# Optimization experiments

Measured on AMD Instinct MI355X. Metric: run time of the kernel, lower is better.

## Reference

```python
import jax, jax.numpy as jnp
import numpy as np

B, T, C, H = 2, 2048, 2048, 16
HD = C // H  # 128


def setup_inputs() -> dict:
    key = jax.random.key(0)
    k1, k2, k3 = jax.random.split(key, 3)
    x = jax.random.normal(k1, (B, T, C), jnp.float32)
    qkv_w = jax.random.normal(k2, (3 * C, C), jnp.float32) / np.float32(np.sqrt(C))
    proj_w = jax.random.normal(k3, (C, C), jnp.float32) / np.float32(np.sqrt(C))
    past = jnp.zeros((B, H, 2, T, HD), jnp.float32)  # KV cache: [B,H,2,max_seq,hd]
    return {"x": x, "qkv_w": qkv_w, "proj_w": proj_w, "past": past, "past_len": 0}


def reference(x, qkv_w, proj_w, past, past_len):
    Bx, Tx, Cx = x.shape
    hd = Cx // H
    # qkv projection (no bias), then split heads: [B,T,3C] -> [B,T,3,H,hd] -> [B,H,T,hd] each
    qkv = jnp.einsum('btc,dc->btd', x, qkv_w).reshape(Bx, Tx, 3, H, hd)
    q = jnp.transpose(qkv[:, :, 0], (0, 2, 1, 3))
    k = jnp.transpose(qkv[:, :, 1], (0, 2, 1, 3))
    v = jnp.transpose(qkv[:, :, 2], (0, 2, 1, 3))
    # KV-cache write (functional scatter) then read back the valid prefix
    past = past.at[:, :, 0, past_len:past_len + Tx].set(k)
    past = past.at[:, :, 1, past_len:past_len + Tx].set(v)
    k = past[:, :, 0, :past_len + Tx]
    v = past[:, :, 1, :past_len + Tx]
    S = past_len + Tx
    scale = np.float32(1.0 / np.sqrt(hd))
    scores = jnp.einsum('bhqd,bhkd->bhqk', q, k) * scale  # [B,H,T,S]
    if Tx > 1:  # is_causal=T>1 in the torch module (past_len=0 on this path)
        mask = jnp.arange(S)[None, :] <= (jnp.arange(Tx)[:, None] + past_len)
        scores = jnp.where(mask, scores, jnp.float32(-jnp.inf))
    attn = jax.nn.softmax(scores, axis=-1)
    out = jnp.einsum('bhqk,bhkd->bhqd', attn, v)  # [B,H,T,hd]
    out = jnp.transpose(out, (0, 2, 1, 3)).reshape(Bx, Tx, Cx)
    return jnp.einsum('btc,dc->btd', out, proj_w)
```

## Files before the change

kernel.cpp:

```cpp
#include <hip/hip_runtime.h>

typedef __bf16 bf16x8 __attribute__((ext_vector_type(8)));
typedef float f32x4 __attribute__((ext_vector_type(4)));
typedef unsigned short u16x8 __attribute__((ext_vector_type(8)));

__device__ __forceinline__ unsigned short f2bf(float f) {
  return __builtin_bit_cast(unsigned short, (__bf16)f);
}

__device__ __forceinline__ void gload16(const void* g, void* l) {
  __builtin_amdgcn_global_load_lds((const __attribute__((address_space(1))) unsigned int*)g,
                                   (__attribute__((address_space(3))) unsigned int*)l,
                                   16, 0, 0);
}

template <int N>
__device__ __forceinline__ float rormax(float x) {
  int r = __builtin_amdgcn_update_dpp(0, __builtin_bit_cast(int, x), 0x120 + N, 0xF, 0xF, true);
  return fmaxf(x, __builtin_bit_cast(float, r));
}
template <int N>
__device__ __forceinline__ float rorsum(float x) {
  int r = __builtin_amdgcn_update_dpp(0, __builtin_bit_cast(int, x), 0x120 + N, 0xF, 0xF, true);
  return x + __builtin_bit_cast(float, r);
}
__device__ __forceinline__ float red16max(float x) {
  x = rormax<8>(x); x = rormax<4>(x); x = rormax<2>(x); return rormax<1>(x);
}
__device__ __forceinline__ float red16sum(float x) {
  x = rorsum<8>(x); x = rorsum<4>(x); x = rorsum<2>(x); return rorsum<1>(x);
}

__global__ __launch_bounds__(256)
void cvt3_f32_bf16(const float* __restrict__ s0, unsigned short* __restrict__ d0, int n0,
                   const float* __restrict__ s1, unsigned short* __restrict__ d1, int n1,
                   const float* __restrict__ s2, unsigned short* __restrict__ d2)
{
  int blk = blockIdx.x;
  const float* s; unsigned short* d;
  if (blk < n0)            { s = s0; d = d0; }
  else if (blk < n0 + n1)  { s = s1; d = d1; blk -= n0; }
  else                     { s = s2; d = d2; blk -= n0 + n1; }
  const size_t e = ((size_t)blk * 256 + threadIdx.x) * 8;
  const float4 a = *(const float4*)(s + e);
  const float4 b = *(const float4*)(s + e + 4);
  u16x8 v;
  v[0] = f2bf(a.x); v[1] = f2bf(a.y); v[2] = f2bf(a.z); v[3] = f2bf(a.w);
  v[4] = f2bf(b.x); v[5] = f2bf(b.y); v[6] = f2bf(b.z); v[7] = f2bf(b.w);
  *(u16x8*)(d + e) = v;
}

#define STG(XS, Xg, buf, half, kt)                                              \
  { gload16((Xg) + (size_t)((half)*128 + srow8) * K + (kt)*64 + scol,           \
            (XS) + (buf)*32768 + (half)*16384 + wid*1024);                      \
    gload16((Xg) + (size_t)((half)*128 + 64 + srow8) * K + (kt)*64 + scol,      \
            (XS) + (buf)*32768 + (half)*16384 + 8192 + wid*1024); }

#define LDA(buf, ih)                                                            \
  { _Pragma("unroll") for (int i = 0; i < 4; ++i) {                             \
      const int ro = (buf)*32768 + arow + ((ih)*64 + i*16)*128;                 \
      af[i][0] = *(const bf16x8*)(As + ro + cbs0);                              \
      af[i][1] = *(const bf16x8*)(As + ro + cbs1); } }

#define LDB(buf, jh, BF)                                                        \
  { _Pragma("unroll") for (int j = 0; j < 2; ++j) {                             \
      const int ro = (buf)*32768 + brow + (((jh)*2 + j)*16)*128;                \
      BF[j][0] = *(const bf16x8*)(Bs + ro + cbs0);                              \
      BF[j][1] = *(const bf16x8*)(Bs + ro + cbs1); } }

#define MM(ih, jh, BF)                                                          \
  { _Pragma("unroll") for (int i = 0; i < 4; ++i)                               \
    _Pragma("unroll") for (int j = 0; j < 2; ++j)                               \
    _Pragma("unroll") for (int kk = 0; kk < 2; ++kk)                            \
      acc[(ih)*4+i][(jh)*2+j] = __builtin_amdgcn_mfma_f32_16x16x32_bf16(        \
          af[i][kk], BF[j][kk], acc[(ih)*4+i][(jh)*2+j], 0, 0, 0); }

#define BAR1_12() { asm volatile("s_waitcnt lgkmcnt(8)" ::: "memory");          \
                    __builtin_amdgcn_s_barrier();                               \
                    asm volatile("s_waitcnt lgkmcnt(0)" ::: "memory");          \
                    __builtin_amdgcn_sched_barrier(0);                          \
                    __builtin_amdgcn_s_setprio(1); }
#define BAR1()    { __builtin_amdgcn_s_barrier();                               \
                    asm volatile("s_waitcnt lgkmcnt(0)" ::: "memory");          \
                    __builtin_amdgcn_sched_barrier(0);                          \
                    __builtin_amdgcn_s_setprio(1); }
#define BAR2()    { __builtin_amdgcn_s_setprio(0); __builtin_amdgcn_s_barrier(); }
#define BAR2V()   { __builtin_amdgcn_s_setprio(0);                              \
                    asm volatile("s_waitcnt vmcnt(4)" ::: "memory");            \
                    __builtin_amdgcn_s_barrier(); }

template <bool OUTBF16>
__global__ __launch_bounds__(512, 1)
void gemm256_bt(const unsigned short* __restrict__ Ap, const unsigned short* __restrict__ Bp,
                void* __restrict__ Outp, int M, int N, int K)
{
  extern __shared__ __align__(16) char smem[];
  char* const As = smem;
  char* const Bs = smem + 65536;
  const int tid = threadIdx.x;
  const int wid = tid >> 6, lane = tid & 63;
  const int wm = wid >> 2, wn = wid & 3;
  const int lg = lane >> 4, lr = lane & 15;

  const int gx = gridDim.x;
  const int nwg = gx * (int)gridDim.y;
  int bid = (int)blockIdx.y * gx + (int)blockIdx.x;
  bid = (bid & 7) * (nwg >> 3) + (bid >> 3);
  const int m0 = (bid / gx) * 256, n0 = (bid % gx) * 256;

  const int srow8 = wid * 8 + (lane >> 3);
  const int scol  = (((lane & 7) ^ (lane >> 3)) << 3);
  const unsigned short* const Ag = Ap + (size_t)m0 * K;
  const unsigned short* const Bg = Bp + (size_t)n0 * K;

  const int cbs0 = (lg * 16) ^ ((lr & 7) << 4);
  const int cbs1 = (64 + lg * 16) ^ ((lr & 7) << 4);
  const int arow = (wm * 128 + lr) * 128;
  const int brow = (wn * 64 + lr) * 128;

  const f32x4 z4 = {0.f, 0.f, 0.f, 0.f};
  f32x4 acc[8][4];
#pragma unroll
  for (int i = 0; i < 8; ++i)
#pragma unroll
    for (int j = 0; j < 4; ++j) acc[i][j] = z4;

  const int NKT = K >> 6;
  bf16x8 af[4][2], bf01[2][2], bf23[2][2];

  STG(As, Ag, 0, 0, 0); STG(As, Ag, 0, 1, 0);
  STG(Bs, Bg, 0, 0, 0); STG(Bs, Bg, 0, 1, 0);
  STG(Bs, Bg, 1, 0, 1); STG(Bs, Bg, 1, 1, 1);
  asm volatile("s_waitcnt vmcnt(4)" ::: "memory");
  __builtin_amdgcn_s_barrier();

  for (int it = 0; it < (NKT >> 1); ++it) {
    const int t1  = 2 * it + 1;
    const int t0n = (2 * it + 2 < NKT) ? 2 * it + 2 : NKT - 1;
    const int t1n = (t1 + 2 < NKT) ? t1 + 2 : NKT - 1;

    LDA(0, 0); LDB(0, 0, bf01); STG(As, Ag, 1, 0, t1);
    BAR1_12(); MM(0, 0, bf01); BAR2();
    LDB(0, 1, bf23); STG(As, Ag, 1, 1, t1);
    BAR1(); MM(0, 1, bf23); BAR2();
    LDA(0, 1); STG(Bs, Bg, 0, 0, t0n);
    BAR1(); MM(1, 0, bf01); BAR2();
    STG(Bs, Bg, 0, 1, t0n);
    BAR1(); MM(1, 1, bf23); BAR2V();
    LDA(1, 0); LDB(1, 0, bf01); STG(As, Ag, 0, 0, t0n);
    BAR1_12(); MM(0, 0, bf01); BAR2();
    LDB(1, 1, bf23); STG(As, Ag, 0, 1, t0n);
    BAR1(); MM(0, 1, bf23); BAR2();
    LDA(1, 1); STG(Bs, Bg, 1, 0, t1n);
    BAR1(); MM(1, 0, bf01); BAR2();
    STG(Bs, Bg, 1, 1, t1n);
    BAR1(); MM(1, 1, bf23); BAR2V();
  }
  asm volatile("s_waitcnt vmcnt(0)" ::: "memory");

#pragma unroll
  for (int i = 0; i < 8; ++i)
#pragma unroll
    for (int j = 0; j < 4; ++j)
#pragma unroll
      for (int r = 0; r < 4; ++r) {
        const int row = m0 + wm * 128 + i * 16 + lg * 4 + r;
        const int col = n0 + wn * 64 + j * 16 + lr;
        const float val = acc[i][j][r];
        if (OUTBF16) ((unsigned short*)Outp)[(size_t)row * N + col] = f2bf(val);
        else         ((float*)Outp)[(size_t)row * N + col] = val;
      }
}

template <bool OUTBF16>
__global__ __launch_bounds__(256, 2)
void gemm_bt16(const unsigned short* __restrict__ Ap, const unsigned short* __restrict__ Bp,
               void* __restrict__ Outp, int M, int N, int K)
{
  __shared__ __align__(16) char smA[128 * 128];
  __shared__ __align__(16) char smB[128 * 128];
  const int tid = threadIdx.x;
  const int wid = tid >> 6, lane = tid & 63;
  const int wr = wid >> 1, wc = wid & 1;
  const int lg = lane >> 4, lr = lane & 15;

  const int gx = gridDim.x;
  const int nwg = gx * gridDim.y;
  int bid = blockIdx.y * gx + blockIdx.x;
  bid = (bid & 7) * (nwg >> 3) + (bid >> 3);
  const int m0 = (bid / gx) * 128, n0 = (bid % gx) * 128;

  const int srow = wid * 8 + (lane >> 3);
  const int scol = (((lane & 7) ^ (lane >> 3)) << 3);
  const int lbase = wid * 1024;

  const f32x4 z4 = {0.f, 0.f, 0.f, 0.f};
  f32x4 acc[4][4];
#pragma unroll
  for (int i = 0; i < 4; ++i)
#pragma unroll
    for (int j = 0; j < 4; ++j) acc[i][j] = z4;

  for (int k0 = 0; k0 < K; k0 += 64) {
    __syncthreads();
#pragma unroll
    for (int c = 0; c < 4; ++c) {
      const int row = c * 32 + srow;
      gload16(Ap + (size_t)(m0 + row) * K + k0 + scol, smA + c * 4096 + lbase);
      gload16(Bp + (size_t)(n0 + row) * K + k0 + scol, smB + c * 4096 + lbase);
    }
    __syncthreads();
#pragma unroll
    for (int kk = 0; kk < 2; ++kk) {
      const int cb = (kk * 32 + lg * 8) * 2;
      bf16x8 a4[4], b4[4];
#pragma unroll
      for (int i = 0; i < 4; ++i) {
        const int row = wr * 64 + i * 16 + lr;
        a4[i] = *(const bf16x8*)(smA + row * 128 + (cb ^ ((row & 7) << 4)));
      }
#pragma unroll
      for (int j = 0; j < 4; ++j) {
        const int row = wc * 64 + j * 16 + lr;
        b4[j] = *(const bf16x8*)(smB + row * 128 + (cb ^ ((row & 7) << 4)));
      }
#pragma unroll
      for (int i = 0; i < 4; ++i)
#pragma unroll
        for (int j = 0; j < 4; ++j)
          acc[i][j] = __builtin_amdgcn_mfma_f32_16x16x32_bf16(a4[i], b4[j], acc[i][j], 0, 0, 0);
    }
  }
#pragma unroll
  for (int i = 0; i < 4; ++i)
#pragma unroll
    for (int j = 0; j < 4; ++j)
#pragma unroll
      for (int r = 0; r < 4; ++r) {
        const int row = m0 + wr * 64 + i * 16 + lg * 4 + r;
        const int col = n0 + wc * 64 + j * 16 + lr;
        const float val = acc[i][j][r];
        if (OUTBF16) ((unsigned short*)Outp)[(size_t)row * N + col] = f2bf(val);
        else         ((float*)Outp)[(size_t)row * N + col] = val;
      }
}

__global__ __launch_bounds__(256)
void vtrans(const unsigned short* __restrict__ qkv, unsigned short* __restrict__ vT)
{
  constexpr int T = 2048, ROWS = 6144;
  const int bh = blockIdx.y, b = bh >> 4, h = bh & 15;
  const int t0 = blockIdx.x * 64;
  const int tid = threadIdx.x;
  __shared__ __align__(16) char Sc[64 * 256];

#pragma unroll
  for (int c = 0; c < 4; ++c) {
    const int row = c * 16 + (tid >> 4);
    const int col = (tid & 15) * 8;
    u16x8 v = *(const u16x8*)(qkv + (size_t)(b * T + t0 + row) * ROWS + 4096 + h * 128 + col);
    *(u16x8*)(Sc + row * 256 + ((col * 2) ^ ((row & 7) << 4))) = v;
  }
  __syncthreads();
#pragma unroll
  for (int c = 0; c < 4; ++c) {
    const int d = c * 32 + (tid >> 3);
    const int t = (tid & 7) * 8;
    u16x8 v;
#pragma unroll
    for (int i = 0; i < 8; ++i)
      v[i] = *(const unsigned short*)(Sc + (t + i) * 256 + ((d * 2) ^ (((t + i) & 7) << 4)));
    *(u16x8*)(vT + ((size_t)bh * 128 + d) * 2048 + t0 + t) = v;
  }
}

__global__ __launch_bounds__(256, 2)
void attn_fwd(const unsigned short* __restrict__ qkv, const unsigned short* __restrict__ vT,
              unsigned short* __restrict__ outp)
{
  constexpr int T = 2048, ROWS = 6144;
  const int blk = blockIdx.x;
  const int qt = 31 - (blk >> 5);
  const int bh = blk & 31;
  const int b = bh >> 4, h = bh & 15;
  const int q0 = qt * 64;
  const int tid = threadIdx.x;
  const int wid = tid >> 6, lane = tid & 63;
  const int lg = lane >> 4, lr = lane & 15;

  __shared__ __align__(16) char Ks[128 * 256];
  __shared__ __align__(16) char Vt[128 * 256];
  __shared__ __align__(16) char Ps[64 * 256];

  const int srow = wid * 4 + (lane >> 4);
  const int scol = (((lane & 15) ^ (srow & 7)) << 3);

  const size_t qrow = (size_t)(b * T + q0 + wid * 16 + lr) * ROWS + h * 128;
  bf16x8 qf[4];
#pragma unroll
  for (int kd = 0; kd < 4; ++kd)
    qf[kd] = __builtin_bit_cast(bf16x8, *(const u16x8*)(qkv + qrow + kd * 32 + lg * 8));

  const f32x4 z4 = {0.f, 0.f, 0.f, 0.f};
  f32x4 oacc[8];
#pragma unroll
  for (int jj = 0; jj < 8; ++jj) oacc[jj] = z4;
  float mrow[4] = {-1e30f, -1e30f, -1e30f, -1e30f};
  float lsum[4] = {0.f, 0.f, 0.f, 0.f};
  const float scale2 = 0.12751745f;

  const int nt = (qt >> 1) + 1;
  for (int kt = 0; kt < nt; ++kt) {
    __syncthreads();
#pragma unroll
    for (int c = 0; c < 8; ++c) {
      gload16(qkv + (size_t)(b * T + kt * 128 + c * 16 + srow) * ROWS + 2048 + h * 128 + scol,
              Ks + c * 4096 + wid * 1024);
      gload16(vT + ((size_t)bh * 128 + c * 16 + srow) * 2048 + kt * 128 + scol,
              Vt + c * 4096 + wid * 1024);
    }
    asm volatile("s_waitcnt vmcnt(0)" ::: "memory");
    __syncthreads();

    f32x4 sf[8];
#pragma unroll
    for (int j = 0; j < 8; ++j) sf[j] = z4;
    __builtin_amdgcn_s_setprio(1);
#pragma unroll
    for (int kd = 0; kd < 4; ++kd) {
      const int cb = (kd * 32 + lg * 8) * 2;
#pragma unroll
      for (int j = 0; j < 8; ++j) {
        const int row = j * 16 + lr;
        bf16x8 kf = *(const bf16x8*)(Ks + row * 256 + (cb ^ ((row & 7) << 4)));
        sf[j] = __builtin_amdgcn_mfma_f32_16x16x32_bf16(qf[kd], kf, sf[j], 0, 0, 0);
      }
    }
    __builtin_amdgcn_s_setprio(0);

    const bool diag = (kt == nt - 1);
#pragma unroll
    for (int j = 0; j < 8; ++j)
#pragma unroll
      for (int r = 0; r < 4; ++r) {
        float s = sf[j][r] * scale2;
        const int key = kt * 128 + j * 16 + lr;
        const int qi  = q0 + wid * 16 + lg * 4 + r;
        if (diag && key > qi) s = -1e30f;
        sf[j][r] = s;
      }
    float pm[4];
#pragma unroll
    for (int r = 0; r < 4; ++r) {
      float m0 = fmaxf(fmaxf(sf[0][r], sf[1][r]), fmaxf(sf[2][r], sf[3][r]));
      float m1 = fmaxf(fmaxf(sf[4][r], sf[5][r]), fmaxf(sf[6][r], sf[7][r]));
      pm[r] = red16max(fmaxf(m0, m1));
    }
    const float growth = fmaxf(fmaxf(pm[0] - mrow[0], pm[1] - mrow[1]),
                               fmaxf(pm[2] - mrow[2], pm[3] - mrow[3]));
    const bool resc = !__all(growth <= 11.5f);
    float alpha[4];
    if (resc) {
#pragma unroll
      for (int r = 0; r < 4; ++r) {
        const float mn = fmaxf(mrow[r], pm[r]);
        alpha[r] = exp2f(mrow[r] - mn);
        mrow[r] = mn;
      }
    }
    float rs[4] = {0.f, 0.f, 0.f, 0.f};
#pragma unroll
    for (int j = 0; j < 8; ++j)
#pragma unroll
      for (int r = 0; r < 4; ++r) {
        const float p = exp2f(sf[j][r] - mrow[r]);
        sf[j][r] = p;
        rs[r] += p;
      }
    if (resc) {
#pragma unroll
      for (int r = 0; r < 4; ++r) lsum[r] = lsum[r] * alpha[r] + red16sum(rs[r]);
    } else {
#pragma unroll
      for (int r = 0; r < 4; ++r) lsum[r] += red16sum(rs[r]);
    }

#pragma unroll
    for (int j = 0; j < 8; ++j)
#pragma unroll
      for (int r = 0; r < 4; ++r) {
        const int prow = wid * 16 + lg * 4 + r;
        const int pcol = j * 16 + lr;
        *(unsigned short*)(Ps + prow * 256 + ((pcol * 2) ^ ((prow & 7) << 4))) = f2bf(sf[j][r]);
      }
    if (resc) {
#pragma unroll
      for (int jj = 0; jj < 8; ++jj)
#pragma unroll
        for (int r = 0; r < 4; ++r) oacc[jj][r] *= alpha[r];
    }
    asm volatile("s_waitcnt lgkmcnt(0)" ::: "memory");
    __builtin_amdgcn_sched_barrier(0);

    __builtin_amdgcn_s_setprio(1);
#pragma unroll
    for (int kk = 0; kk < 4; ++kk) {
      const int prow = wid * 16 + lr;
      const int pcb = (kk * 32 + lg * 8) * 2;
      bf16x8 pf = *(const bf16x8*)(Ps + prow * 256 + (pcb ^ ((prow & 7) << 4)));
#pragma unroll
      for (int jj = 0; jj < 8; ++jj) {
        const int vrow = jj * 16 + lr;
        bf16x8 vf = *(const bf16x8*)(Vt + vrow * 256 + (pcb ^ ((vrow & 7) << 4)));
        oacc[jj] = __builtin_amdgcn_mfma_f32_16x16x32_bf16(pf, vf, oacc[jj], 0, 0, 0);
      }
    }
    __builtin_amdgcn_s_setprio(0);
  }

#pragma unroll
  for (int jj = 0; jj < 8; ++jj)
#pragma unroll
    for (int r = 0; r < 4; ++r) {
      const int q = q0 + wid * 16 + lg * 4 + r;
      const int col = h * 128 + jj * 16 + lr;
      const float o = oacc[jj][r] / lsum[r];
      outp[(size_t)(b * T + q) * 2048 + col] = f2bf(o);
    }
}

extern "C" void kernel_launch(void* const* d_in, const int* in_sizes, int n_in,
                              void* d_out, int out_size, void* d_ws, size_t ws_size,
                              hipStream_t stream) {
  (void)in_sizes; (void)n_in; (void)out_size; (void)ws_size;
  const float* x     = (const float*)d_in[0];
  const float* qkvw  = (const float*)d_in[1];
  const float* projw = (const float*)d_in[2];

  unsigned short* qkvb   = (unsigned short*)d_ws;
  unsigned short* attnb  = qkvb   + (size_t)4096 * 6144;
  unsigned short* xb     = attnb  + (size_t)4096 * 2048;
  unsigned short* qkvwb  = xb     + (size_t)4096 * 2048;
  unsigned short* projwb = qkvwb  + (size_t)6144 * 2048;
  unsigned short* vT     = xb;
  float* out = (float*)d_out;

  static bool attr_set = false;
  if (!attr_set) {
    hipFuncSetAttribute((const void*)gemm256_bt<true>,
                        hipFuncAttributeMaxDynamicSharedMemorySize, 131072);
    attr_set = true;
  }

  cvt3_f32_bf16<<<4096 + 6144 + 2048, 256, 0, stream>>>(
      x, xb, 4096, qkvw, qkvwb, 6144, projw, projwb);
  gemm256_bt<true><<<dim3(6144 / 256, 4096 / 256), 512, 131072, stream>>>(
      xb, qkvwb, qkvb, 4096, 6144, 2048);
  vtrans<<<dim3(32, 32), 256, 0, stream>>>(qkvb, vT);
  attn_fwd<<<1024, 256, 0, stream>>>(qkvb, vT, attnb);
  gemm_bt16<false><<<dim3(2048 / 128, 4096 / 128), 256, 0, stream>>>(
      attnb, projwb, out, 4096, 2048, 2048);
}
```

Before: 255.0 us.

## Retile QKV GEMM to 256x192 tiles for even wave count

Replaces the 256x256 QKV projection GEMM with a 256x192 tile variant so the grid becomes 32x16 workgroups, which should remove the partial last wave on the GPU. B staging, LDS buffers, register fragments and the MFMA schedule are restructured for three 64-row B chunks per k-step, with the vmcnt waits adjusted to match. Narrower tiles lower arithmetic intensity per workgroup and add more A reloads in exchange.

```diff
diff --git a/kernel.cpp b/kernel.cpp
--- a/kernel.cpp
+++ b/kernel.cpp
@@ -50,30 +50,45 @@
   *(u16x8*)(d + e) = v;
 }
 
-#define STG(XS, Xg, buf, half, kt)                                              \
-  { gload16((Xg) + (size_t)((half)*128 + srow8) * K + (kt)*64 + scol,           \
-            (XS) + (buf)*32768 + (half)*16384 + wid*1024);                      \
-    gload16((Xg) + (size_t)((half)*128 + 64 + srow8) * K + (kt)*64 + scol,      \
-            (XS) + (buf)*32768 + (half)*16384 + 8192 + wid*1024); }
-
-#define LDA(buf, ih)                                                            \
+#define SA(buf, half, kt)                                                       \
+  { gload16(Ag + (size_t)((half)*128 + srow8) * K + (kt)*64 + scol,             \
+            As + (buf)*32768 + (half)*16384 + wid*1024);                        \
+    gload16(Ag + (size_t)((half)*128 + 64 + srow8) * K + (kt)*64 + scol,        \
+            As + (buf)*32768 + (half)*16384 + 8192 + wid*1024); }
+
+#define SB(buf, u, kt)                                                          \
+  { gload16(Bg + (size_t)((u)*64 + srow8) * K + (kt)*64 + scol,                 \
+            Bs + (buf)*24576 + (u)*8192 + wid*1024); }
+
+#define LA(buf, ih)                                                             \
   { _Pragma("unroll") for (int i = 0; i < 4; ++i) {                             \
       const int ro = (buf)*32768 + arow + ((ih)*64 + i*16)*128;                 \
       af[i][0] = *(const bf16x8*)(As + ro + cbs0);                              \
       af[i][1] = *(const bf16x8*)(As + ro + cbs1); } }
 
-#define LDB(buf, jh, BF)                                                        \
+#define LB2(buf)                                                                \
   { _Pragma("unroll") for (int j = 0; j < 2; ++j) {                             \
-      const int ro = (buf)*32768 + brow + (((jh)*2 + j)*16)*128;                \
-      BF[j][0] = *(const bf16x8*)(Bs + ro + cbs0);                              \
-      BF[j][1] = *(const bf16x8*)(Bs + ro + cbs1); } }
-
-#define MM(ih, jh, BF)                                                          \
+      const int ro = (buf)*24576 + brow + j*2048;                               \
+      B2[j][0] = *(const bf16x8*)(Bs + ro + cbs0);                              \
+      B2[j][1] = *(const bf16x8*)(Bs + ro + cbs1); } }
+
+#define LB1(buf)                                                                \
+  { const int ro = (buf)*24576 + brow + 4096;                                   \
+    B1[0] = *(const bf16x8*)(Bs + ro + cbs0);                                   \
+    B1[1] = *(const bf16x8*)(Bs + ro + cbs1); }
+
+#define M2(ih)                                                                  \
   { _Pragma("unroll") for (int i = 0; i < 4; ++i)                               \
     _Pragma("unroll") for (int j = 0; j < 2; ++j)                               \
     _Pragma("unroll") for (int kk = 0; kk < 2; ++kk)                            \
-      acc[(ih)*4+i][(jh)*2+j] = __builtin_amdgcn_mfma_f32_16x16x32_bf16(        \
-          af[i][kk], BF[j][kk], acc[(ih)*4+i][(jh)*2+j], 0, 0, 0); }
+      acc[(ih)*4+i][j] = __builtin_amdgcn_mfma_f32_16x16x32_bf16(               \
+          af[i][kk], B2[j][kk], acc[(ih)*4+i][j], 0, 0, 0); }
+
+#define M1(ih)                                                                  \
+  { _Pragma("unroll") for (int i = 0; i < 4; ++i)                               \
+    _Pragma("unroll") for (int kk = 0; kk < 2; ++kk)                            \
+      acc[(ih)*4+i][2] = __builtin_amdgcn_mfma_f32_16x16x32_bf16(               \
+          af[i][kk], B1[kk], acc[(ih)*4+i][2], 0, 0, 0); }
 
 #define BAR1_12() { asm volatile("s_waitcnt lgkmcnt(8)" ::: "memory");          \
                     __builtin_amdgcn_s_barrier();                               \
@@ -85,14 +100,13 @@
                     __builtin_amdgcn_sched_barrier(0);                          \
                     __builtin_amdgcn_s_setprio(1); }
 #define BAR2()    { __builtin_amdgcn_s_setprio(0); __builtin_amdgcn_s_barrier(); }
-#define BAR2V()   { __builtin_amdgcn_s_setprio(0);                              \
-                    asm volatile("s_waitcnt vmcnt(4)" ::: "memory");            \
+#define BAR2V3()  { __builtin_amdgcn_s_setprio(0);                              \
+                    asm volatile("s_waitcnt vmcnt(3)" ::: "memory");            \
                     __builtin_amdgcn_s_barrier(); }
 
-template <bool OUTBF16>
 __global__ __launch_bounds__(512, 1)
-void gemm256_bt(const unsigned short* __restrict__ Ap, const unsigned short* __restrict__ Bp,
-                void* __restrict__ Outp, int M, int N, int K)
+void gemm_n192(const unsigned short* __restrict__ Ap, const unsigned short* __restrict__ Bp,
+               unsigned short* __restrict__ Outp, int M, int N, int K)
 {
   extern __shared__ __align__(16) char smem[];
   char* const As = smem;
@@ -106,7 +120,7 @@
   const int nwg = gx * (int)gridDim.y;
   int bid = (int)blockIdx.y * gx + (int)blockIdx.x;
   bid = (bid & 7) * (nwg >> 3) + (bid >> 3);
-  const int m0 = (bid / gx) * 256, n0 = (bid % gx) * 256;
+  const int m0 = (bid / gx) * 256, n0 = (bid % gx) * 192;
 
   const int srow8 = wid * 8 + (lane >> 3);
   const int scol  = (((lane & 7) ^ (lane >> 3)) << 3);
@@ -116,22 +130,22 @@
   const int cbs0 = (lg * 16) ^ ((lr & 7) << 4);
   const int cbs1 = (64 + lg * 16) ^ ((lr & 7) << 4);
   const int arow = (wm * 128 + lr) * 128;
-  const int brow = (wn * 64 + lr) * 128;
+  const int brow = (wn * 48 + lr) * 128;
 
   const f32x4 z4 = {0.f, 0.f, 0.f, 0.f};
-  f32x4 acc[8][4];
+  f32x4 acc[8][3];
 #pragma unroll
   for (int i = 0; i < 8; ++i)
 #pragma unroll
-    for (int j = 0; j < 4; ++j) acc[i][j] = z4;
+    for (int j = 0; j < 3; ++j) acc[i][j] = z4;
 
   const int NKT = K >> 6;
-  bf16x8 af[4][2], bf01[2][2], bf23[2][2];
-
-  STG(As, Ag, 0, 0, 0); STG(As, Ag, 0, 1, 0);
-  STG(Bs, Bg, 0, 0, 0); STG(Bs, Bg, 0, 1, 0);
-  STG(Bs, Bg, 1, 0, 1); STG(Bs, Bg, 1, 1, 1);
-  asm volatile("s_waitcnt vmcnt(4)" ::: "memory");
+  bf16x8 af[4][2], B2[2][2], B1[2];
+
+  SA(0, 0, 0); SA(0, 1, 0);
+  SB(0, 0, 0); SB(0, 1, 0); SB(0, 2, 0);
+  SB(1, 0, 1); SB(1, 1, 1); SB(1, 2, 1);
+  asm volatile("s_waitcnt vmcnt(3)" ::: "memory");
   __builtin_amdgcn_s_barrier();
 
   for (int it = 0; it < (NKT >> 1); ++it) {
@@ -139,38 +153,40 @@
     const int t0n = (2 * it + 2 < NKT) ? 2 * it + 2 : NKT - 1;
     const int t1n = (t1 + 2 < NKT) ? t1 + 2 : NKT - 1;
 
-    LDA(0, 0); LDB(0, 0, bf01); STG(As, Ag, 1, 0, t1);
-    BAR1_12(); MM(0, 0, bf01); BAR2();
-    LDB(0, 1, bf23); STG(As, Ag, 1, 1, t1);
-    BAR1(); MM(0, 1, bf23); BAR2();
-    LDA(0, 1); STG(Bs, Bg, 0, 0, t0n);
-    BAR1(); MM(1, 0, bf01); BAR2();
-    STG(Bs, Bg, 0, 1, t0n);
-    BAR1(); MM(1, 1, bf23); BAR2V();
-    LDA(1, 0); LDB(1, 0, bf01); STG(As, Ag, 0, 0, t0n);
-    BAR1_12(); MM(0, 0, bf01); BAR2();
-    LDB(1, 1, bf23); STG(As, Ag, 0, 1, t0n);
-    BAR1(); MM(0, 1, bf23); BAR2();
-    LDA(1, 1); STG(Bs, Bg, 1, 0, t1n);
-    BAR1(); MM(1, 0, bf01); BAR2();
-    STG(Bs, Bg, 1, 1, t1n);
-    BAR1(); MM(1, 1, bf23); BAR2V();
+    LA(0, 0); LB2(0); SA(1, 0, t1);
+    BAR1_12(); M2(0); BAR2();
+    LB1(0); SA(1, 1, t1);
+    BAR1(); M1(0); BAR2();
+    LA(0, 1); SB(0, 0, t0n); SB(0, 1, t0n);
+    BAR1(); M2(1); BAR2();
+    SB(0, 2, t0n);
+    BAR1(); M1(1); BAR2V3();
+    LA(1, 0); LB2(1); SA(0, 0, t0n);
+    BAR1_12(); M2(0); BAR2();
+    LB1(1); SA(0, 1, t0n);
+    BAR1(); M1(0); BAR2();
+    LA(1, 1); SB(1, 0, t1n); SB(1, 1, t1n);
+    BAR1(); M2(1); BAR2();
+    SB(1, 2, t1n);
+    BAR1(); M1(1); BAR2V3();
   }
   asm volatile("s_waitcnt vmcnt(0)" ::: "memory");
 
 #pragma unroll
   for (int i = 0; i < 8; ++i)
 #pragma unroll
-    for (int j = 0; j < 4; ++j)
+    for (int j = 0; j < 3; ++j)
 #pragma unroll
       for (int r = 0; r < 4; ++r) {
         const int row = m0 + wm * 128 + i * 16 + lg * 4 + r;
-        const int col = n0 + wn * 64 + j * 16 + lr;
-        const float val = acc[i][j][r];
-        if (OUTBF16) ((unsigned short*)Outp)[(size_t)row * N + col] = f2bf(val);
-        else         ((float*)Outp)[(size_t)row * N + col] = val;
-      }
-}
+        const int col = n0 + wn * 48 + j * 16 + lr;
+        Outp[(size_t)row * N + col] = f2bf(acc[i][j][r]);
+      }
+}
+
+#define GSTG(XS, Xg, c)                                                         \
+  gload16((Xg) + (size_t)(m_or_n + (c)*32 + srow) * K + k0 + scol,              \
+          (XS) + (c)*4096 + lbase)
 
 template <bool OUTBF16>
 __global__ __launch_bounds__(256, 2)
@@ -447,14 +463,14 @@
 
   static bool attr_set = false;
   if (!attr_set) {
-    hipFuncSetAttribute((const void*)gemm256_bt<true>,
-                        hipFuncAttributeMaxDynamicSharedMemorySize, 131072);
+    hipFuncSetAttribute((const void*)gemm_n192,
+                        hipFuncAttributeMaxDynamicSharedMemorySize, 114688);
     attr_set = true;
   }
 
   cvt3_f32_bf16<<<4096 + 6144 + 2048, 256, 0, stream>>>(
       x, xb, 4096, qkvw, qkvwb, 6144, projw, projwb);
-  gemm256_bt<true><<<dim3(6144 / 256, 4096 / 256), 512, 131072, stream>>>(
+  gemm_n192<<<dim3(6144 / 192, 4096 / 256), 512, 114688, stream>>>(
       xb, qkvwb, qkvb, 4096, 6144, 2048);
   vtrans<<<dim3(32, 32), 256, 0, stream>>>(qkvb, vT);
   attn_fwd<<<1024, 256, 0, stream>>>(qkvb, vT, attnb);
```

New measurement: 253.1 us. Within noise of the previous version (-0.7%).
